# Kernel tuning notes

Measured on AMD Instinct MI355X. Metric: run time of the kernel, lower is better.

The kernel has to match this reference:

```python
import jax, jax.numpy as jnp
import numpy as np

N_NODES = 100000
N_EDGES = 1600000
IN_C, HID_C, OUT_C = 128, 64, 64


def setup_inputs() -> dict:
    key = jax.random.key(0)
    ks = jax.random.split(key, 9)
    x = jax.random.normal(ks[0], (N_NODES, IN_C), dtype=jnp.float32)
    src = jax.random.randint(ks[1], (N_EDGES,), 0, N_NODES, dtype=jnp.int64)
    dst = jax.random.randint(ks[2], (N_EDGES,), 0, N_NODES, dtype=jnp.int64)
    # Glorot-ish init for linear weights
    W1 = jax.random.normal(ks[3], (IN_C, HID_C), dtype=jnp.float32) / np.sqrt(IN_C)
    b1 = jnp.zeros((HID_C,), dtype=jnp.float32)
    W2 = jax.random.normal(ks[4], (HID_C, HID_C), dtype=jnp.float32) / np.sqrt(HID_C)
    b2 = jnp.zeros((HID_C,), dtype=jnp.float32)
    W3 = jax.random.normal(ks[5], (HID_C, OUT_C), dtype=jnp.float32) / np.sqrt(HID_C)
    b3 = jnp.zeros((OUT_C,), dtype=jnp.float32)
    return {"x": x, "src": src, "dst": dst,
            "W1": W1, "b1": b1, "W2": W2, "b2": b2, "W3": W3, "b3": b3}


def _gcn_conv(x, src, dst, W, b):
    # GCNConv(normalize=False): out = A @ (x W) + b  (unweighted sum aggregation)
    h = x @ W                          # [N, d_out] dense transform first (d_out small)
    msg = h[src]                       # gather per edge: [E, d_out]
    agg = jax.ops.segment_sum(msg, dst, num_segments=N_NODES)  # scatter-add
    return agg + b


def reference(x, src, dst, W1, b1, W2, b2, W3, b3):
    # layer 1..num_layers-1: conv -> activation -> dropout(eval: no-op)
    h = jax.nn.relu(_gcn_conv(x, src, dst, W1, b1))
    h = jax.nn.relu(_gcn_conv(h, src, dst, W2, b2))
    # last layer: conv -> activation
    out = jax.nn.relu(_gcn_conv(h, src, dst, W3, b3))
    return out
```

## Files before the change

kernel.cpp:

```cpp
#include <hip/hip_runtime.h>

#define N_NODES_C 100000
#define N_EDGES_C 1600000
#define NPB 256
#define CH (N_EDGES_C / NPB)
#define BUCK_SH 7
#define BUCK_NODES 128
#define NB_BUCK 782

typedef short short8 __attribute__((ext_vector_type(8)));
typedef float f32x4 __attribute__((ext_vector_type(4)));

__device__ __forceinline__ short f2bf(float f) {
  unsigned u = __builtin_bit_cast(unsigned, f);
  unsigned r = (u + 0x7FFFu + ((u >> 16) & 1u)) >> 16;
  return (short)r;
}
__device__ __forceinline__ float bf_lo(unsigned u) {
  return __builtin_bit_cast(float, u << 16);
}
__device__ __forceinline__ float bf_hi(unsigned u) {
  return __builtin_bit_cast(float, u & 0xFFFF0000u);
}

template <int K, bool IN_BF, bool OUT_BF>
__device__ __forceinline__ void gemm64_body(
    int gblock, const void* __restrict__ in_, const float* __restrict__ W,
    void* __restrict__ out_, int n_rows) {
  constexpr int KS = K / 32;
  int wave = threadIdx.x >> 6;
  int lane = threadIdx.x & 63;
  int row0 = (gblock * 4 + wave) * 16;
  if (row0 >= n_rows) return;

  int lrow = lane & 15;
  int lk = (lane >> 4) * 8;

  short8 bfrag[KS][4];
#pragma unroll
  for (int ks = 0; ks < KS; ++ks)
#pragma unroll
    for (int nt = 0; nt < 4; ++nt) {
      short8 b;
#pragma unroll
      for (int j = 0; j < 8; ++j)
        b[j] = f2bf(W[(size_t)(ks * 32 + lk + j) * 64 + nt * 16 + lrow]);
      bfrag[ks][nt] = b;
    }

  int row = row0 + lrow;
  f32x4 acc[4] = {};
#pragma unroll
  for (int ks = 0; ks < KS; ++ks) {
    short8 a;
    if constexpr (IN_BF) {
      const short* ip = (const short*)in_ + (size_t)row * K + ks * 32 + lk;
      a = *(const short8*)ip;
    } else {
      const float* ip = (const float*)in_ + (size_t)row * K + ks * 32 + lk;
      f32x4 v0 = *(const f32x4*)(ip);
      f32x4 v1 = *(const f32x4*)(ip + 4);
#pragma unroll
      for (int j = 0; j < 4; ++j) {
        a[j] = f2bf(v0[j]);
        a[4 + j] = f2bf(v1[j]);
      }
    }
#pragma unroll
    for (int nt = 0; nt < 4; ++nt)
      acc[nt] = __builtin_amdgcn_mfma_f32_16x16x32_bf16(a, bfrag[ks][nt],
                                                        acc[nt], 0, 0, 0);
  }

  int crow = row0 + (lane >> 4) * 4;
#pragma unroll
  for (int nt = 0; nt < 4; ++nt) {
    int ocol = nt * 16 + lrow;
#pragma unroll
    for (int r = 0; r < 4; ++r) {
      if constexpr (OUT_BF)
        ((short*)out_)[(size_t)(crow + r) * 64 + ocol] = f2bf(acc[nt][r]);
      else
        ((float*)out_)[(size_t)(crow + r) * 64 + ocol] = acc[nt][r];
    }
  }
}

__global__ __launch_bounds__(256) void hist_kernel(
    const int* __restrict__ dst, int* __restrict__ countsT) {
  __shared__ int lhist[NB_BUCK];
  int cb = (int)blockIdx.x;
  for (int i = threadIdx.x; i < NB_BUCK; i += 256) lhist[i] = 0;
  __syncthreads();
  int beg = cb * CH, end = beg + CH;
  for (int i = beg + (int)threadIdx.x; i < end; i += 256)
    atomicAdd(&lhist[((unsigned)dst[i]) >> BUCK_SH], 1);
  __syncthreads();
  for (int bb = threadIdx.x; bb < NB_BUCK; bb += 256)
    countsT[bb * NPB + cb] = lhist[bb];
}

__global__ __launch_bounds__(256) void scan_buckets_kernel(
    int* __restrict__ countsT, int* __restrict__ btot) {
  int b = blockIdx.x * 4 + (threadIdx.x >> 6);
  int lane = threadIdx.x & 63;
  if (b >= NB_BUCK) return;
  int4 v = *(const int4*)(countsT + b * NPB + lane * 4);
  int s = v.x + v.y + v.z + v.w;
  int incl = s;
#pragma unroll
  for (int d = 1; d < 64; d <<= 1) {
    int t = __shfl_up(incl, d, 64);
    if (lane >= d) incl += t;
  }
  int excl = incl - s;
  int4 o;
  o.x = excl;
  o.y = excl + v.x;
  o.z = o.y + v.y;
  o.w = o.z + v.z;
  *(int4*)(countsT + b * NPB + lane * 4) = o;
  if (lane == 63) btot[b] = incl;
}

__global__ __launch_bounds__(1024) void scan_btot_kernel(
    const int* __restrict__ btot, int* __restrict__ bstart) {
  __shared__ int lds[1024];
  int t = threadIdx.x;
  int v = (t < NB_BUCK) ? btot[t] : 0;
  lds[t] = v;
  __syncthreads();
  for (int off = 1; off < 1024; off <<= 1) {
    int tv = (t >= off) ? lds[t - off] : 0;
    __syncthreads();
    lds[t] += tv;
    __syncthreads();
  }
  if (t < NB_BUCK) bstart[t] = lds[t] - v;
  if (t == NB_BUCK - 1) bstart[NB_BUCK] = lds[t];
}

__global__ __launch_bounds__(256) void part_gemm1_kernel(
    const int* __restrict__ src, const int* __restrict__ dst,
    const int* __restrict__ offs ,
    const int* __restrict__ bstart, unsigned* __restrict__ packed,
    const float* __restrict__ x, const float* __restrict__ W1,
    short* __restrict__ hA, int n_rows) {
  __shared__ int cur[NB_BUCK];
  int b = (int)blockIdx.x;
  if (b >= NPB) {
    gemm64_body<128, false, true>(b - NPB, x, W1, hA, n_rows);
    return;
  }
  for (int bb = threadIdx.x; bb < NB_BUCK; bb += 256)
    cur[bb] = bstart[bb] + offs[bb * NPB + b];
  __syncthreads();
  int beg = b * CH, end = beg + CH;
  for (int i = beg + (int)threadIdx.x; i < end; i += 256) {
    int d = dst[i];
    int s = src[i];
    int bb = ((unsigned)d) >> BUCK_SH;
    int pos = atomicAdd(&cur[bb], 1);
    packed[pos] = ((unsigned)(d & (BUCK_NODES - 1)) << 17) | (unsigned)s;
  }
}

__global__ __launch_bounds__(256) void sort_bucket_kernel(
    const unsigned* __restrict__ packed, const int* __restrict__ bstart,
    int* __restrict__ col, int* __restrict__ row_ptr, int n_nodes,
    int n_edges) {
  __shared__ int lhist[BUCK_NODES];
  __shared__ int lcur[BUCK_NODES];
  __shared__ int wsum0;
  int b = (int)blockIdx.x;
  int beg = bstart[b], end = bstart[b + 1];
  int t = (int)threadIdx.x;

  if (t < BUCK_NODES) lhist[t] = 0;
  __syncthreads();
  for (int e = beg + t; e < end; e += 256)
    atomicAdd(&lhist[packed[e] >> 17], 1);
  __syncthreads();

  int v = 0, incl = 0;
  if (t < BUCK_NODES) {
    v = lhist[t];
    incl = v;
#pragma unroll
    for (int d = 1; d < 64; d <<= 1) {
      int u = __shfl_up(incl, d, 64);
      if ((t & 63) >= d) incl += u;
    }
  }
  if (t == 63) wsum0 = incl;
  __syncthreads();
  if (t >= 64 && t < BUCK_NODES) incl += wsum0;
  if (t < BUCK_NODES) {
    int excl = incl - v;
    lcur[t] = excl;
    int node = b * BUCK_NODES + t;
    if (node < n_nodes) row_ptr[node] = beg + excl;
  }
  if (b == NB_BUCK - 1 && t == 0) row_ptr[n_nodes] = n_edges;
  __syncthreads();

  for (int e = beg + t; e < end; e += 256) {
    unsigned pe = packed[e];
    int ld = (int)(pe >> 17);
    int pos = beg + atomicAdd(&lcur[ld], 1);
    col[pos] = (int)(pe & 0x1FFFFu);
  }
}

__device__ __forceinline__ void agg_node(
    const short* __restrict__ h, const int* __restrict__ col, int beg, int end,
    int slot, int q, float& s0, float& s1, float& s2, float& s3) {
  s0 = s1 = s2 = s3 = 0.f;
  float t0 = 0.f, t1 = 0.f, t2 = 0.f, t3 = 0.f;
  int e = beg + slot;
  for (; e + 12 < end; e += 16) {
    int sa = col[e];
    int sb = col[e + 4];
    int sc = col[e + 8];
    int sd = col[e + 12];
    uint2 ua = *(const uint2*)(h + (size_t)sa * 64 + q * 4);
    uint2 ub = *(const uint2*)(h + (size_t)sb * 64 + q * 4);
    uint2 uc = *(const uint2*)(h + (size_t)sc * 64 + q * 4);
    uint2 ud = *(const uint2*)(h + (size_t)sd * 64 + q * 4);
    s0 += bf_lo(ua.x) + bf_lo(ub.x);
    s1 += bf_hi(ua.x) + bf_hi(ub.x);
    s2 += bf_lo(ua.y) + bf_lo(ub.y);
    s3 += bf_hi(ua.y) + bf_hi(ub.y);
    t0 += bf_lo(uc.x) + bf_lo(ud.x);
    t1 += bf_hi(uc.x) + bf_hi(ud.x);
    t2 += bf_lo(uc.y) + bf_lo(ud.y);
    t3 += bf_hi(uc.y) + bf_hi(ud.y);
  }
  for (; e < end; e += 4) {
    int sa = col[e];
    uint2 ua = *(const uint2*)(h + (size_t)sa * 64 + q * 4);
    s0 += bf_lo(ua.x);
    s1 += bf_hi(ua.x);
    s2 += bf_lo(ua.y);
    s3 += bf_hi(ua.y);
  }
  s0 += t0;
  s1 += t1;
  s2 += t2;
  s3 += t3;
  s0 += __shfl_xor(s0, 16);
  s1 += __shfl_xor(s1, 16);
  s2 += __shfl_xor(s2, 16);
  s3 += __shfl_xor(s3, 16);
  s0 += __shfl_xor(s0, 32);
  s1 += __shfl_xor(s1, 32);
  s2 += __shfl_xor(s2, 32);
  s3 += __shfl_xor(s3, 32);
}

__global__ __launch_bounds__(256) void agg_gemm_kernel(
    const short* __restrict__ h, const int* __restrict__ row_ptr,
    const int* __restrict__ col, const float* __restrict__ bias,
    const float* __restrict__ W, short* __restrict__ outg, int n_nodes) {
  __shared__ float rowbuf[16][68];
  int wid = threadIdx.x >> 6;
  int lane = threadIdx.x & 63;
  int slot = lane >> 4;
  int q = lane & 15;
  int nbase = blockIdx.x * 16;

#pragma unroll
  for (int n = 0; n < 4; ++n) {
    int ln = wid * 4 + n;
    int node = nbase + ln;
    float s0, s1, s2, s3;
    agg_node(h, col, row_ptr[node], row_ptr[node + 1], slot, q, s0, s1, s2, s3);
    if (lane < 16) {
      f32x4 r;
      r[0] = fmaxf(s0 + bias[q * 4 + 0], 0.f);
      r[1] = fmaxf(s1 + bias[q * 4 + 1], 0.f);
      r[2] = fmaxf(s2 + bias[q * 4 + 2], 0.f);
      r[3] = fmaxf(s3 + bias[q * 4 + 3], 0.f);
      *(f32x4*)&rowbuf[ln][q * 4] = r;
    }
  }
  __syncthreads();

  int lrow = lane & 15;
  int lk = (lane >> 4) * 8;
  f32x4 acc = {};
#pragma unroll
  for (int ks = 0; ks < 2; ++ks) {
    short8 a, bv;
#pragma unroll
    for (int j = 0; j < 8; ++j) a[j] = f2bf(rowbuf[lrow][ks * 32 + lk + j]);
#pragma unroll
    for (int j = 0; j < 8; ++j)
      bv[j] = f2bf(W[(size_t)(ks * 32 + lk + j) * 64 + wid * 16 + lrow]);
    acc = __builtin_amdgcn_mfma_f32_16x16x32_bf16(a, bv, acc, 0, 0, 0);
  }
  int crow = (lane >> 4) * 4;
#pragma unroll
  for (int r = 0; r < 4; ++r)
    outg[(size_t)(nbase + crow + r) * 64 + wid * 16 + lrow] = f2bf(acc[r]);
}

__global__ __launch_bounds__(256) void agg_final_kernel(
    const short* __restrict__ h, const int* __restrict__ row_ptr,
    const int* __restrict__ col, const float* __restrict__ bias,
    float* __restrict__ out, int n_nodes) {
  int node = blockIdx.x * 4 + (threadIdx.x >> 6);
  if (node >= n_nodes) return;
  int lane = threadIdx.x & 63;
  int slot = lane >> 4;
  int q = lane & 15;
  float s0, s1, s2, s3;
  agg_node(h, col, row_ptr[node], row_ptr[node + 1], slot, q, s0, s1, s2, s3);
  if (lane < 16) {
    float4 v;
    v.x = fmaxf(s0 + bias[q * 4 + 0], 0.f);
    v.y = fmaxf(s1 + bias[q * 4 + 1], 0.f);
    v.z = fmaxf(s2 + bias[q * 4 + 2], 0.f);
    v.w = fmaxf(s3 + bias[q * 4 + 3], 0.f);
    ((float4*)out)[(size_t)node * 16 + q] = v;
  }
}

extern "C" void kernel_launch(void* const* d_in, const int* in_sizes, int n_in,
                              void* d_out, int out_size, void* d_ws,
                              size_t ws_size, hipStream_t stream) {
  const float* x = (const float*)d_in[0];
  const int* src = (const int*)d_in[1];
  const int* dst = (const int*)d_in[2];
  const float* W1 = (const float*)d_in[3];
  const float* b1 = (const float*)d_in[4];
  const float* W2 = (const float*)d_in[5];
  const float* b2 = (const float*)d_in[6];
  const float* W3 = (const float*)d_in[7];
  const float* b3 = (const float*)d_in[8];
  float* out = (float*)d_out;

  const int N = N_NODES_C;
  const int E = N_EDGES_C;

  char* ws = (char*)d_ws;
  int* countsT = (int*)(ws + 0);
  int* btot = (int*)(ws + (1u << 20));
  int* bstart = (int*)(ws + (1u << 20) + (16u << 10));
  int* row_ptr = (int*)(ws + (2u << 20));
  unsigned* packed = (unsigned*)(ws + (3u << 20));
  int* col = (int*)(ws + (10u << 20));
  short* hA = (short*)(ws + (17u << 20));
  short* hB = (short*)(ws + (30u << 20));

  const int gemm_grid = (N + 63) / 64;
  const int k1_grid = (NB_BUCK + 3) / 4;
  const int aggg_grid = N / 16;
  const int aggf_grid = (N + 3) / 4;

  hist_kernel<<<NPB, 256, 0, stream>>>(dst, countsT);
  scan_buckets_kernel<<<k1_grid, 256, 0, stream>>>(countsT, btot);
  scan_btot_kernel<<<1, 1024, 0, stream>>>(btot, bstart);
  part_gemm1_kernel<<<NPB + gemm_grid, 256, 0, stream>>>(
      src, dst, countsT, bstart, packed, x, W1, hA, N);
  sort_bucket_kernel<<<NB_BUCK, 256, 0, stream>>>(packed, bstart, col, row_ptr,
                                                  N, E);

  agg_gemm_kernel<<<aggg_grid, 256, 0, stream>>>(hA, row_ptr, col, b1, W2, hB,
                                                 N);
  agg_gemm_kernel<<<aggg_grid, 256, 0, stream>>>(hB, row_ptr, col, b2, W3, hA,
                                                 N);
  agg_final_kernel<<<aggf_grid, 256, 0, stream>>>(hA, row_ptr, col, b3, out, N);
}
```

Before: 213.4 us.

## Move layer-1 GEMM from partition kernel into bucket-sort kernel, halve partition blocks

Cuts the number of partition/histogram blocks from 256 to 128 and adapts the per-bucket scan to two counts per lane. The first-layer dense GEMM blocks move out of the partition kernel and are appended to the bucket-sort launch, so they co-run with the sort instead of the partition. This rebalances which CSR-construction phase hides the GEMM. Fewer partition blocks mean fewer LDS atomic streams and a smaller counts table, but each block does twice as much serial work.

```diff
diff --git a/kernel.cpp b/kernel.cpp
--- a/kernel.cpp
+++ b/kernel.cpp
@@ -2,7 +2,7 @@
 
 #define N_NODES_C 100000
 #define N_EDGES_C 1600000
-#define NPB 256
+#define NPB 128
 #define CH (N_EDGES_C / NPB)
 #define BUCK_SH 7
 #define BUCK_NODES 128
@@ -105,8 +105,8 @@
   int b = blockIdx.x * 4 + (threadIdx.x >> 6);
   int lane = threadIdx.x & 63;
   if (b >= NB_BUCK) return;
-  int4 v = *(const int4*)(countsT + b * NPB + lane * 4);
-  int s = v.x + v.y + v.z + v.w;
+  int2 v = *(const int2*)(countsT + b * NPB + lane * 2);
+  int s = v.x + v.y;
   int incl = s;
 #pragma unroll
   for (int d = 1; d < 64; d <<= 1) {
@@ -114,12 +114,10 @@
     if (lane >= d) incl += t;
   }
   int excl = incl - s;
-  int4 o;
+  int2 o;
   o.x = excl;
   o.y = excl + v.x;
-  o.z = o.y + v.y;
-  o.w = o.z + v.z;
-  *(int4*)(countsT + b * NPB + lane * 4) = o;
+  *(int2*)(countsT + b * NPB + lane * 2) = o;
   if (lane == 63) btot[b] = incl;
 }
 
@@ -140,18 +138,12 @@
   if (t == NB_BUCK - 1) bstart[NB_BUCK] = lds[t];
 }
 
-__global__ __launch_bounds__(256) void part_gemm1_kernel(
+__global__ __launch_bounds__(256) void partition_kernel(
     const int* __restrict__ src, const int* __restrict__ dst,
     const int* __restrict__ offs ,
-    const int* __restrict__ bstart, unsigned* __restrict__ packed,
-    const float* __restrict__ x, const float* __restrict__ W1,
-    short* __restrict__ hA, int n_rows) {
+    const int* __restrict__ bstart, unsigned* __restrict__ packed) {
   __shared__ int cur[NB_BUCK];
   int b = (int)blockIdx.x;
-  if (b >= NPB) {
-    gemm64_body<128, false, true>(b - NPB, x, W1, hA, n_rows);
-    return;
-  }
   for (int bb = threadIdx.x; bb < NB_BUCK; bb += 256)
     cur[bb] = bstart[bb] + offs[bb * NPB + b];
   __syncthreads();
@@ -165,14 +157,19 @@
   }
 }
 
-__global__ __launch_bounds__(256) void sort_bucket_kernel(
+__global__ __launch_bounds__(256) void sort_gemm1_kernel(
     const unsigned* __restrict__ packed, const int* __restrict__ bstart,
     int* __restrict__ col, int* __restrict__ row_ptr, int n_nodes,
-    int n_edges) {
+    int n_edges, const float* __restrict__ x, const float* __restrict__ W1,
+    short* __restrict__ hA) {
   __shared__ int lhist[BUCK_NODES];
   __shared__ int lcur[BUCK_NODES];
   __shared__ int wsum0;
   int b = (int)blockIdx.x;
+  if (b >= NB_BUCK) {
+    gemm64_body<128, false, true>(b - NB_BUCK, x, W1, hA, n_nodes);
+    return;
+  }
   int beg = bstart[b], end = bstart[b + 1];
   int t = (int)threadIdx.x;
 
@@ -361,10 +358,9 @@
   hist_kernel<<<NPB, 256, 0, stream>>>(dst, countsT);
   scan_buckets_kernel<<<k1_grid, 256, 0, stream>>>(countsT, btot);
   scan_btot_kernel<<<1, 1024, 0, stream>>>(btot, bstart);
-  part_gemm1_kernel<<<NPB + gemm_grid, 256, 0, stream>>>(
-      src, dst, countsT, bstart, packed, x, W1, hA, N);
-  sort_bucket_kernel<<<NB_BUCK, 256, 0, stream>>>(packed, bstart, col, row_ptr,
-                                                  N, E);
+  partition_kernel<<<NPB, 256, 0, stream>>>(src, dst, countsT, bstart, packed);
+  sort_gemm1_kernel<<<NB_BUCK + gemm_grid, 256, 0, stream>>>(
+      packed, bstart, col, row_ptr, N, E, x, W1, hA);
 
   agg_gemm_kernel<<<aggg_grid, 256, 0, stream>>>(hA, row_ptr, col, b1, W2, hB,
                                                  N);
```

Result: slower. 220.6 us (+3.4%).

## Store hidden features as FP8 E4M3 and halve partition block count

Applied to the files above, without the earlier changes.

Intermediate node features are stored as 8-bit E4M3 values with a software encoder and decoder instead of bf16, halving the bytes moved by the random per-edge gathers in the aggregation kernels. Separately, the partition pass now uses 128 blocks over 256 histogram chunks, each reading the offset of every second chunk, so each block scatters a larger range. The FP8 format loses precision (three mantissa bits, small values flush to zero, large values clamp), which may exceed the tolerance. The software decode also adds several integer ops per element.

```diff
diff --git a/kernel.cpp b/kernel.cpp
--- a/kernel.cpp
+++ b/kernel.cpp
@@ -2,8 +2,10 @@
 
 #define N_NODES_C 100000
 #define N_EDGES_C 1600000
-#define NPB 256
-#define CH (N_EDGES_C / NPB)
+#define NCHUNK 256
+#define CHH (N_EDGES_C / NCHUNK)
+#define NPART 128
+#define CHP (N_EDGES_C / NPART)
 #define BUCK_SH 7
 #define BUCK_NODES 128
 #define NB_BUCK 782
@@ -16,17 +18,27 @@
   unsigned r = (u + 0x7FFFu + ((u >> 16) & 1u)) >> 16;
   return (short)r;
 }
-__device__ __forceinline__ float bf_lo(unsigned u) {
-  return __builtin_bit_cast(float, u << 16);
-}
-__device__ __forceinline__ float bf_hi(unsigned u) {
-  return __builtin_bit_cast(float, u & 0xFFFF0000u);
-}
-
-template <int K, bool IN_BF, bool OUT_BF>
+
+__device__ __forceinline__ float fp8_to_f32(unsigned b) {
+  unsigned f = ((b & 0x80u) << 24) | (((b & 0x7Fu) + 0x3C0u) << 20);
+  return (b & 0x78u) ? __builtin_bit_cast(float, f) : 0.f;
+}
+__device__ __forceinline__ unsigned f32_to_fp8(float x) {
+  unsigned u = __builtin_bit_cast(unsigned, x);
+  unsigned s = (u >> 24) & 0x80u;
+  unsigned au = u & 0x7FFFFFFFu;
+  if (au < (121u << 23)) return s;
+  unsigned r = au + 0x7FFFFu + ((au >> 20) & 1u);
+  unsigned e8 = (r >> 23) - 120u;
+  unsigned m = (r >> 20) & 7u;
+  if (e8 > 15u) { e8 = 15u; m = 6u; }
+  return s | (e8 << 3) | m;
+}
+
+template <int K>
 __device__ __forceinline__ void gemm64_body(
-    int gblock, const void* __restrict__ in_, const float* __restrict__ W,
-    void* __restrict__ out_, int n_rows) {
+    int gblock, const float* __restrict__ in_, const float* __restrict__ W,
+    unsigned char* __restrict__ out_, int n_rows) {
   constexpr int KS = K / 32;
   int wave = threadIdx.x >> 6;
   int lane = threadIdx.x & 63;
@@ -53,18 +65,13 @@
 #pragma unroll
   for (int ks = 0; ks < KS; ++ks) {
     short8 a;
-    if constexpr (IN_BF) {
-      const short* ip = (const short*)in_ + (size_t)row * K + ks * 32 + lk;
-      a = *(const short8*)ip;
-    } else {
-      const float* ip = (const float*)in_ + (size_t)row * K + ks * 32 + lk;
-      f32x4 v0 = *(const f32x4*)(ip);
-      f32x4 v1 = *(const f32x4*)(ip + 4);
-#pragma unroll
-      for (int j = 0; j < 4; ++j) {
-        a[j] = f2bf(v0[j]);
-        a[4 + j] = f2bf(v1[j]);
-      }
+    const float* ip = in_ + (size_t)row * K + ks * 32 + lk;
+    f32x4 v0 = *(const f32x4*)(ip);
+    f32x4 v1 = *(const f32x4*)(ip + 4);
+#pragma unroll
+    for (int j = 0; j < 4; ++j) {
+      a[j] = f2bf(v0[j]);
+      a[4 + j] = f2bf(v1[j]);
     }
 #pragma unroll
     for (int nt = 0; nt < 4; ++nt)
@@ -77,12 +84,8 @@
   for (int nt = 0; nt < 4; ++nt) {
     int ocol = nt * 16 + lrow;
 #pragma unroll
-    for (int r = 0; r < 4; ++r) {
-      if constexpr (OUT_BF)
-        ((short*)out_)[(size_t)(crow + r) * 64 + ocol] = f2bf(acc[nt][r]);
-      else
-        ((float*)out_)[(size_t)(crow + r) * 64 + ocol] = acc[nt][r];
-    }
+    for (int r = 0; r < 4; ++r)
+      out_[(size_t)(crow + r) * 64 + ocol] = (unsigned char)f32_to_fp8(acc[nt][r]);
   }
 }
 
@@ -92,12 +95,12 @@
   int cb = (int)blockIdx.x;
   for (int i = threadIdx.x; i < NB_BUCK; i += 256) lhist[i] = 0;
   __syncthreads();
-  int beg = cb * CH, end = beg + CH;
+  int beg = cb * CHH, end = beg + CHH;
   for (int i = beg + (int)threadIdx.x; i < end; i += 256)
     atomicAdd(&lhist[((unsigned)dst[i]) >> BUCK_SH], 1);
   __syncthreads();
   for (int bb = threadIdx.x; bb < NB_BUCK; bb += 256)
-    countsT[bb * NPB + cb] = lhist[bb];
+    countsT[bb * NCHUNK + cb] = lhist[bb];
 }
 
 __global__ __launch_bounds__(256) void scan_buckets_kernel(
@@ -105,7 +108,7 @@
   int b = blockIdx.x * 4 + (threadIdx.x >> 6);
   int lane = threadIdx.x & 63;
   if (b >= NB_BUCK) return;
-  int4 v = *(const int4*)(countsT + b * NPB + lane * 4);
+  int4 v = *(const int4*)(countsT + b * NCHUNK + lane * 4);
   int s = v.x + v.y + v.z + v.w;
   int incl = s;
 #pragma unroll
@@ -119,7 +122,7 @@
   o.y = excl + v.x;
   o.z = o.y + v.y;
   o.w = o.z + v.z;
-  *(int4*)(countsT + b * NPB + lane * 4) = o;
+  *(int4*)(countsT + b * NCHUNK + lane * 4) = o;
   if (lane == 63) btot[b] = incl;
 }
 
@@ -145,17 +148,17 @@
     const int* __restrict__ offs ,
     const int* __restrict__ bstart, unsigned* __restrict__ packed,
     const float* __restrict__ x, const float* __restrict__ W1,
-    short* __restrict__ hA, int n_rows) {
+    unsigned char* __restrict__ hA, int n_rows) {
   __shared__ int cur[NB_BUCK];
   int b = (int)blockIdx.x;
-  if (b >= NPB) {
-    gemm64_body<128, false, true>(b - NPB, x, W1, hA, n_rows);
+  if (b >= NPART) {
+    gemm64_body<128>(b - NPART, x, W1, hA, n_rows);
     return;
   }
   for (int bb = threadIdx.x; bb < NB_BUCK; bb += 256)
-    cur[bb] = bstart[bb] + offs[bb * NPB + b];
-  __syncthreads();
-  int beg = b * CH, end = beg + CH;
+    cur[bb] = bstart[bb] + offs[bb * NCHUNK + 2 * b];
+  __syncthreads();
+  int beg = b * CHP, end = beg + CHP;
   for (int i = beg + (int)threadIdx.x; i < end; i += 256) {
     int d = dst[i];
     int s = src[i];
@@ -213,8 +216,8 @@
 }
 
 __device__ __forceinline__ void agg_node(
-    const short* __restrict__ h, const int* __restrict__ col, int beg, int end,
-    int slot, int q, float& s0, float& s1, float& s2, float& s3) {
+    const unsigned char* __restrict__ h, const int* __restrict__ col, int beg,
+    int end, int slot, int q, float& s0, float& s1, float& s2, float& s3) {
   s0 = s1 = s2 = s3 = 0.f;
   float t0 = 0.f, t1 = 0.f, t2 = 0.f, t3 = 0.f;
   int e = beg + slot;
@@ -223,26 +226,26 @@
     int sb = col[e + 4];
     int sc = col[e + 8];
     int sd = col[e + 12];
-    uint2 ua = *(const uint2*)(h + (size_t)sa * 64 + q * 4);
-    uint2 ub = *(const uint2*)(h + (size_t)sb * 64 + q * 4);
-    uint2 uc = *(const uint2*)(h + (size_t)sc * 64 + q * 4);
-    uint2 ud = *(const uint2*)(h + (size_t)sd * 64 + q * 4);
-    s0 += bf_lo(ua.x) + bf_lo(ub.x);
-    s1 += bf_hi(ua.x) + bf_hi(ub.x);
-    s2 += bf_lo(ua.y) + bf_lo(ub.y);
-    s3 += bf_hi(ua.y) + bf_hi(ub.y);
-    t0 += bf_lo(uc.x) + bf_lo(ud.x);
-    t1 += bf_hi(uc.x) + bf_hi(ud.x);
-    t2 += bf_lo(uc.y) + bf_lo(ud.y);
-    t3 += bf_hi(uc.y) + bf_hi(ud.y);
+    unsigned ua = *(const unsigned*)(h + (size_t)sa * 64 + q * 4);
+    unsigned ub = *(const unsigned*)(h + (size_t)sb * 64 + q * 4);
+    unsigned uc = *(const unsigned*)(h + (size_t)sc * 64 + q * 4);
+    unsigned ud = *(const unsigned*)(h + (size_t)sd * 64 + q * 4);
+    s0 += fp8_to_f32(ua & 255u) + fp8_to_f32(ub & 255u);
+    s1 += fp8_to_f32((ua >> 8) & 255u) + fp8_to_f32((ub >> 8) & 255u);
+    s2 += fp8_to_f32((ua >> 16) & 255u) + fp8_to_f32((ub >> 16) & 255u);
+    s3 += fp8_to_f32(ua >> 24) + fp8_to_f32(ub >> 24);
+    t0 += fp8_to_f32(uc & 255u) + fp8_to_f32(ud & 255u);
+    t1 += fp8_to_f32((uc >> 8) & 255u) + fp8_to_f32((ud >> 8) & 255u);
+    t2 += fp8_to_f32((uc >> 16) & 255u) + fp8_to_f32((ud >> 16) & 255u);
+    t3 += fp8_to_f32(uc >> 24) + fp8_to_f32(ud >> 24);
   }
   for (; e < end; e += 4) {
     int sa = col[e];
-    uint2 ua = *(const uint2*)(h + (size_t)sa * 64 + q * 4);
-    s0 += bf_lo(ua.x);
-    s1 += bf_hi(ua.x);
-    s2 += bf_lo(ua.y);
-    s3 += bf_hi(ua.y);
+    unsigned ua = *(const unsigned*)(h + (size_t)sa * 64 + q * 4);
+    s0 += fp8_to_f32(ua & 255u);
+    s1 += fp8_to_f32((ua >> 8) & 255u);
+    s2 += fp8_to_f32((ua >> 16) & 255u);
+    s3 += fp8_to_f32(ua >> 24);
   }
   s0 += t0;
   s1 += t1;
@@ -259,9 +262,10 @@
 }
 
 __global__ __launch_bounds__(256) void agg_gemm_kernel(
-    const short* __restrict__ h, const int* __restrict__ row_ptr,
+    const unsigned char* __restrict__ h, const int* __restrict__ row_ptr,
     const int* __restrict__ col, const float* __restrict__ bias,
-    const float* __restrict__ W, short* __restrict__ outg, int n_nodes) {
+    const float* __restrict__ W, unsigned char* __restrict__ outg,
+    int n_nodes) {
   __shared__ float rowbuf[16][68];
   int wid = threadIdx.x >> 6;
   int lane = threadIdx.x & 63;
@@ -302,11 +306,12 @@
   int crow = (lane >> 4) * 4;
 #pragma unroll
   for (int r = 0; r < 4; ++r)
-    outg[(size_t)(nbase + crow + r) * 64 + wid * 16 + lrow] = f2bf(acc[r]);
+    outg[(size_t)(nbase + crow + r) * 64 + wid * 16 + lrow] =
+        (unsigned char)f32_to_fp8(acc[r]);
 }
 
 __global__ __launch_bounds__(256) void agg_final_kernel(
-    const short* __restrict__ h, const int* __restrict__ row_ptr,
+    const unsigned char* __restrict__ h, const int* __restrict__ row_ptr,
     const int* __restrict__ col, const float* __restrict__ bias,
     float* __restrict__ out, int n_nodes) {
   int node = blockIdx.x * 4 + (threadIdx.x >> 6);
@@ -350,18 +355,18 @@
   int* row_ptr = (int*)(ws + (2u << 20));
   unsigned* packed = (unsigned*)(ws + (3u << 20));
   int* col = (int*)(ws + (10u << 20));
-  short* hA = (short*)(ws + (17u << 20));
-  short* hB = (short*)(ws + (30u << 20));
+  unsigned char* hA = (unsigned char*)(ws + (17u << 20));
+  unsigned char* hB = (unsigned char*)(ws + (24u << 20));
 
   const int gemm_grid = (N + 63) / 64;
   const int k1_grid = (NB_BUCK + 3) / 4;
   const int aggg_grid = N / 16;
   const int aggf_grid = (N + 3) / 4;
 
-  hist_kernel<<<NPB, 256, 0, stream>>>(dst, countsT);
+  hist_kernel<<<NCHUNK, 256, 0, stream>>>(dst, countsT);
   scan_buckets_kernel<<<k1_grid, 256, 0, stream>>>(countsT, btot);
   scan_btot_kernel<<<1, 1024, 0, stream>>>(btot, bstart);
-  part_gemm1_kernel<<<NPB + gemm_grid, 256, 0, stream>>>(
+  part_gemm1_kernel<<<NPART + gemm_grid, 256, 0, stream>>>(
       src, dst, countsT, bstart, packed, x, W1, hA, N);
   sort_bucket_kernel<<<NB_BUCK, 256, 0, stream>>>(packed, bstart, col, row_ptr,
                                                   N, E);
```

Measured after the change: 248.4 us. +16.4%, slower.
